# Optimization experiments

Measured on AMD Instinct MI355X. Metric: run time of the kernel, lower is better.

The kernel has to match this reference:

```python
import jax, jax.numpy as jnp
import numpy as np

NEG_INF = -9e15
LEAKY_SLOPE = 0.2  # init alpha
N, IN_DIM, OUT_DIM = 8192, 512, 256


def setup_inputs() -> dict:
    key = jax.random.key(0)
    k1, k2, k3, k4, k5 = jax.random.split(key, 5)
    h = jax.random.normal(k1, (N, IN_DIM), dtype=jnp.float32)
    adj = jax.random.randint(k2, (N, N), 0, 2, dtype=jnp.int32)
    W = jax.random.normal(k3, (IN_DIM, OUT_DIM), dtype=jnp.float32) * 0.06
    a_left = jax.random.normal(k4, (OUT_DIM, 1), dtype=jnp.float32) * 0.1
    a_right = jax.random.normal(k5, (OUT_DIM, 1), dtype=jnp.float32) * 0.1
    return {"h": h, "adj": adj, "W": W, "a_left": a_left, "a_right": a_right}


def reference(h, adj, W, a_left, a_right):
    Wh = h @ W                                  # [N, out_dim]
    Wh1 = Wh @ a_left                           # [N, 1]
    Wh2 = Wh @ a_right                          # [N, 1]
    e = Wh1 + Wh2.T                             # [N, N] broadcast additive scores
    e = jnp.where(e > 0, e, LEAKY_SLOPE * e)    # LeakyReLU
    e = jnp.where(adj > 0, e, NEG_INF)          # adjacency mask
    attention = jax.nn.softmax(e, axis=1)       # row-wise softmax (dropout=0, eval)
    h_out = attention @ Wh                      # [N, out_dim]
    return jax.nn.elu(h_out)                    # activation=True
```

## Files before the change

kernel.cpp:

```cpp
#include <hip/hip_runtime.h>
#include <hip/hip_bf16.h>
#include <cstdint>
#include <cstddef>

typedef float  f32x4  __attribute__((ext_vector_type(4)));
typedef __bf16 bf16x8 __attribute__((ext_vector_type(8)));

#define LOG2E 1.4426950408889634f

static constexpr int GN   = 8192;
static constexpr int GIN  = 512;
static constexpr int GOUT = 256;

static __device__ __forceinline__ void gload_lds16(const void* g, void* lds){
  typedef uint32_t __attribute__((address_space(1)))* gp_t;
  typedef uint32_t __attribute__((address_space(3)))* lp_t;
  __builtin_amdgcn_global_load_lds((gp_t)(uintptr_t)g,
                                   (lp_t)(uint32_t)(uintptr_t)lds, 16, 0, 0);
}

__global__ void k_wa(const float* __restrict__ W, const float* __restrict__ al,
                     const float* __restrict__ ar, float* __restrict__ wal,
                     float* __restrict__ war){
  int k = blockIdx.x;
  int lane = threadIdx.x;
  float4 wv = ((const float4*)(W + (size_t)k*GOUT))[lane];
  float4 av = ((const float4*)al)[lane];
  float4 bv = ((const float4*)ar)[lane];
  float sl = wv.x*av.x + wv.y*av.y + wv.z*av.z + wv.w*av.w;
  float sr = wv.x*bv.x + wv.y*bv.y + wv.z*bv.z + wv.w*bv.w;
  #pragma unroll
  for(int o=32;o;o>>=1){ sl += __shfl_down(sl,o,64); sr += __shfl_down(sr,o,64); }
  if(lane==0){ wal[k] = sl*LOG2E; war[k] = sr*LOG2E; }
}

__global__ void k_prep_h(const float* __restrict__ h, const float* __restrict__ wal,
                         const float* __restrict__ war, __bf16* __restrict__ hb,
                         float* __restrict__ Wh1, float* __restrict__ Wh2){
  int row = blockIdx.x*4 + (threadIdx.x>>6);
  int lane = threadIdx.x & 63;
  const float4* hp = (const float4*)(h + (size_t)row*GIN);
  float4 v0 = hp[lane*2], v1 = hp[lane*2+1];
  bf16x8 o;
  o[0]=(__bf16)v0.x; o[1]=(__bf16)v0.y; o[2]=(__bf16)v0.z; o[3]=(__bf16)v0.w;
  o[4]=(__bf16)v1.x; o[5]=(__bf16)v1.y; o[6]=(__bf16)v1.z; o[7]=(__bf16)v1.w;
  *(bf16x8*)(hb + (size_t)row*GIN + lane*8) = o;
  float4 a0 = ((const float4*)wal)[lane*2], a1 = ((const float4*)wal)[lane*2+1];
  float4 b0 = ((const float4*)war)[lane*2], b1 = ((const float4*)war)[lane*2+1];
  float sl = v0.x*a0.x+v0.y*a0.y+v0.z*a0.z+v0.w*a0.w
           + v1.x*a1.x+v1.y*a1.y+v1.z*a1.z+v1.w*a1.w;
  float sr = v0.x*b0.x+v0.y*b0.y+v0.z*b0.z+v0.w*b0.w
           + v1.x*b1.x+v1.y*b1.y+v1.z*b1.z+v1.w*b1.w;
  #pragma unroll
  for(int of=32;of;of>>=1){ sl += __shfl_down(sl,of,64); sr += __shfl_down(sr,of,64); }
  if(lane==0){ Wh1[row]=sl; Wh2[row]=sr; }
}

__global__ void k_wt(const float* __restrict__ W, __bf16* __restrict__ WT){
  int idx = blockIdx.x*256 + threadIdx.x;
  int k = idx >> 8, c = idx & 255;
  WT[(size_t)c*GIN + k] = (__bf16)W[idx];
}

__global__ __launch_bounds__(256,1) void k_gemmT(const __bf16* __restrict__ WT,
                                                 const __bf16* __restrict__ hb,
                                                 __bf16* __restrict__ WhbT){
  __shared__ __attribute__((aligned(16))) __bf16 As[2][64*64];
  __shared__ __attribute__((aligned(16))) __bf16 Bs[2][128*64];
  const int tid = threadIdx.x, lane = tid & 63, w = tid >> 6;
  const int mb = blockIdx.x >> 6, nb = blockIdx.x & 63;
  const int m0 = mb*64, n0 = nb*128;

  f32x4 acc[8];
  #pragma unroll
  for(int t=0;t<8;t++) acc[t] = (f32x4){0.f,0.f,0.f,0.f};

  const int lr = lane>>3;
  const int bs_sw = ((lane&7)*16) ^ (lr<<4);

  auto stage = [&](int it, int buf){
    const int k0b = it*128;
    #pragma unroll
    for(int s=0;s<6;s++){
      int u = w + s*4;
      const char* src; char* dst;
      if(u < 8){
        int r8 = u*8;
        src = (const char*)(WT + (size_t)(m0 + r8 + lr)*GIN);
        dst = (char*)&As[buf][0] + r8*128;
      } else {
        int r8 = (u-8)*8;
        src = (const char*)(hb + (size_t)(n0 + r8 + lr)*GIN);
        dst = (char*)&Bs[buf][0] + r8*128;
      }
      gload_lds16(src + k0b + bs_sw, dst);
    }
  };

  auto kstep = [&](int kk, int buf){
    const int ko = kk*64 + (lane>>4)*16;
    const int am = 16*w + (lane&15);
    bf16x8 af = *(const bf16x8*)((const char*)&As[buf][0] + am*128 + (ko ^ ((am&7)<<4)));
    #pragma unroll
    for(int t=0;t<8;t++){
      int n = 16*t + (lane&15);
      bf16x8 bf = *(const bf16x8*)((const char*)&Bs[buf][0] + n*128 + (ko ^ ((n&7)<<4)));
      acc[t] = __builtin_amdgcn_mfma_f32_16x16x32_bf16(af, bf, acc[t], 0, 0, 0);
    }
  };

  stage(0,0);
  asm volatile("s_waitcnt vmcnt(0)" ::: "memory");
  __builtin_amdgcn_s_barrier();
  for(int it=0; it<8; it++){
    int buf = it & 1;
    if(it < 7) stage(it+1, buf^1);
    kstep(0, buf);
    kstep(1, buf);
    asm volatile("s_waitcnt vmcnt(0)" ::: "memory");
    __builtin_amdgcn_s_barrier();
  }

  const int mrow = m0 + 16*w + 4*(lane>>4);
  const int nc0  = n0 + (lane&15);
  #pragma unroll
  for(int t=0;t<8;t++){
    #pragma unroll
    for(int r=0;r<4;r++){
      WhbT[(size_t)(mrow + r)*GN + nc0 + 16*t] = (__bf16)acc[t][r];
    }
  }
}

template<bool PART>
__global__ __launch_bounds__(256,2) void k_attn(const int* __restrict__ adj,
                                                const __bf16* __restrict__ WhbT,
                                                const float* __restrict__ Wh1s,
                                                const float* __restrict__ Wh2s,
                                                float* __restrict__ pv_out,
                                                float* __restrict__ s_out){
  __shared__ __attribute__((aligned(16))) __bf16 Vs[2][256*64];
  const int tid = threadIdx.x, lane = tid & 63, w = tid >> 6;
  const int rg = blockIdx.x >> 3, chunk = blockIdx.x & 7;
  const int r0 = rg * 128;
  const int j0 = chunk * 1024;

  f32x4 acc0[16], acc1[16];
  #pragma unroll
  for(int t=0;t<16;t++){ acc0[t] = (f32x4){0.f,0.f,0.f,0.f}; acc1[t] = (f32x4){0.f,0.f,0.f,0.f}; }
  f32x4 accs0 = (f32x4){0.f,0.f,0.f,0.f};
  f32x4 accs1 = (f32x4){0.f,0.f,0.f,0.f};

  bf16x8 ones;
  #pragma unroll
  for(int j=0;j<8;j++) ones[j] = (__bf16)1.0f;

  const int kg  = lane >> 4;
  const int kg8 = kg << 3;
  const int myrow0 = r0 + 16*w + (lane & 15);
  const float wh1_0 = Wh1s[myrow0];
  const float wh1_1 = Wh1s[myrow0 + 64];
  const float* wh2p = Wh2s + j0 + kg8;

  const size_t arow0 = (size_t)(r0 + 16*w) * GN + j0;
  const size_t arow1 = arow0 + (size_t)64 * GN;

  const int lr = lane>>3;
  const int bs_sw = ((lane&7)*16) ^ (lr<<4);

  auto stage = [&](int it, int buf){
    const int colb = (j0 + it*64)*2;
    #pragma unroll
    for(int s=0;s<8;s++){
      int u = w + s*4;
      int r8 = u*8;
      const char* src = (const char*)WhbT + (size_t)(r8 + lr)*(GN*2) + colb + bs_sw;
      gload_lds16(src, (char*)&Vs[buf][0] + r8*128);
    }
  };

  int a0p[16], a1p[16];
  auto adj_load = [&](int tt){
    const int co = tt*64 + lane;
    #pragma unroll
    for(int r=0;r<16;r++) a0p[r] = adj[arow0 + (size_t)r*GN + co];
    #pragma unroll
    for(int r=0;r<16;r++) a1p[r] = adj[arow1 + (size_t)r*GN + co];
  };
  auto adj_pack = [&](uint64_t& m0, uint64_t& m1){
    uint64_t n0 = 0, n1 = 0;
    #pragma unroll
    for(int r=0;r<16;r++){
      uint64_t b = __ballot(a0p[r] != 0);
      if((lane&15)==r) n0 = b;
    }
    #pragma unroll
    for(int r=0;r<16;r++){
      uint64_t b = __ballot(a1p[r] != 0);
      if((lane&15)==r) n1 = b;
    }
    m0 = n0; m1 = n1;
  };

  auto mkpa = [&](float wh1, unsigned m8, float4 w0, float4 w1) -> bf16x8 {
    bf16x8 pa;
    float y, p;
    y = wh1 + w0.x; y = fmaxf(y, 0.2f*y); p = exp2f(y); pa[0] = (__bf16)((m8    )&1 ? p : 0.f);
    y = wh1 + w0.y; y = fmaxf(y, 0.2f*y); p = exp2f(y); pa[1] = (__bf16)((m8>>1)&1 ? p : 0.f);
    y = wh1 + w0.z; y = fmaxf(y, 0.2f*y); p = exp2f(y); pa[2] = (__bf16)((m8>>2)&1 ? p : 0.f);
    y = wh1 + w0.w; y = fmaxf(y, 0.2f*y); p = exp2f(y); pa[3] = (__bf16)((m8>>3)&1 ? p : 0.f);
    y = wh1 + w1.x; y = fmaxf(y, 0.2f*y); p = exp2f(y); pa[4] = (__bf16)((m8>>4)&1 ? p : 0.f);
    y = wh1 + w1.y; y = fmaxf(y, 0.2f*y); p = exp2f(y); pa[5] = (__bf16)((m8>>5)&1 ? p : 0.f);
    y = wh1 + w1.z; y = fmaxf(y, 0.2f*y); p = exp2f(y); pa[6] = (__bf16)((m8>>6)&1 ? p : 0.f);
    y = wh1 + w1.w; y = fmaxf(y, 0.2f*y); p = exp2f(y); pa[7] = (__bf16)((m8>>7)&1 ? p : 0.f);
    return pa;
  };

  uint64_t mk0, mk1;

  auto kstep = [&](int it, int kk, int buf){
    const float* wp = wh2p + it*64 + kk*32;
    float4 w0 = *(const float4*)wp;
    float4 w1 = *(const float4*)(wp + 4);
    unsigned m8_0 = (unsigned)((mk0 >> (kk*32 + kg8)) & 0xffULL);
    unsigned m8_1 = (unsigned)((mk1 >> (kk*32 + kg8)) & 0xffULL);
    bf16x8 pa0 = mkpa(wh1_0, m8_0, w0, w1);
    bf16x8 pa1 = mkpa(wh1_1, m8_1, w0, w1);
    const int ko = kk*64 + kg*16;
    #pragma unroll
    for(int t=0;t<16;t++){
      int n = 16*t + (lane&15);
      bf16x8 bv = *(const bf16x8*)((const char*)&Vs[buf][0] + n*128 + (ko ^ ((n&7)<<4)));
      acc0[t] = __builtin_amdgcn_mfma_f32_16x16x32_bf16(pa0, bv, acc0[t], 0, 0, 0);
      acc1[t] = __builtin_amdgcn_mfma_f32_16x16x32_bf16(pa1, bv, acc1[t], 0, 0, 0);
    }
    accs0 = __builtin_amdgcn_mfma_f32_16x16x32_bf16(pa0, ones, accs0, 0, 0, 0);
    accs1 = __builtin_amdgcn_mfma_f32_16x16x32_bf16(pa1, ones, accs1, 0, 0, 0);
  };

  stage(0, 0);
  adj_load(0);
  adj_pack(mk0, mk1);
  asm volatile("s_waitcnt vmcnt(0)" ::: "memory");
  __builtin_amdgcn_s_barrier();

  for(int it=0; it<16; it++){
    int buf = it & 1;
    if(it < 15){
      stage(it+1, buf^1);
      adj_load(it+1);
    }
    kstep(it, 0, buf);
    kstep(it, 1, buf);
    uint64_t mkn0 = 0, mkn1 = 0;
    if(it < 15) adj_pack(mkn0, mkn1);
    asm volatile("s_waitcnt vmcnt(0)" ::: "memory");
    __builtin_amdgcn_s_barrier();
    mk0 = mkn0; mk1 = mkn1;
  }

  const int orow0 = r0 + 16*w + 4*kg;
  const int orow1 = orow0 + 64;
  const int ocol  = lane & 15;
  if constexpr (PART){
    float* pv = pv_out + (size_t)chunk*GN*GOUT;
    float* sp = s_out  + (size_t)chunk*GN;
    #pragma unroll
    for(int t=0;t<16;t++){
      #pragma unroll
      for(int r=0;r<4;r++){
        pv[(size_t)(orow0 + r)*GOUT + ocol + 16*t] = acc0[t][r];
        pv[(size_t)(orow1 + r)*GOUT + ocol + 16*t] = acc1[t][r];
      }
    }
    if(ocol == 0){
      #pragma unroll
      for(int r=0;r<4;r++){ sp[orow0 + r] = accs0[r]; sp[orow1 + r] = accs1[r]; }
    }
  } else {
    #pragma unroll
    for(int t=0;t<16;t++){
      #pragma unroll
      for(int r=0;r<4;r++){
        atomicAdd(pv_out + (size_t)(orow0 + r)*GOUT + ocol + 16*t, acc0[t][r]);
        atomicAdd(pv_out + (size_t)(orow1 + r)*GOUT + ocol + 16*t, acc1[t][r]);
      }
    }
    if(ocol == 0){
      #pragma unroll
      for(int r=0;r<4;r++){ atomicAdd(s_out + orow0 + r, accs0[r]); atomicAdd(s_out + orow1 + r, accs1[r]); }
    }
  }
}

static __device__ __forceinline__ float elu1(float x){
  return x > 0.f ? x : (exp2f(x*LOG2E) - 1.f);
}

__global__ void k_reduce(const float* __restrict__ accP, const float* __restrict__ accSp,
                         float* __restrict__ out){
  size_t i = ((size_t)blockIdx.x*256 + threadIdx.x)*4;
  int row = (int)(i >> 8);
  float S = 0.f;
  #pragma unroll
  for(int c=0;c<8;c++) S += accSp[(size_t)c*GN + row];
  float4 s = {0.f,0.f,0.f,0.f};
  #pragma unroll
  for(int c=0;c<8;c++){
    float4 v = *(const float4*)(accP + (size_t)c*GN*GOUT + i);
    s.x += v.x; s.y += v.y; s.z += v.z; s.w += v.w;
  }
  float inv = 1.0f / S;
  float4 o;
  o.x = elu1(s.x*inv); o.y = elu1(s.y*inv); o.z = elu1(s.z*inv); o.w = elu1(s.w*inv);
  *(float4*)(out + i) = o;
}

__global__ void k_norm(const float* __restrict__ accPV, const float* __restrict__ accS,
                       float* __restrict__ out){
  size_t i = ((size_t)blockIdx.x*256 + threadIdx.x)*4;
  int row = (int)(i >> 8);
  float inv = 1.0f / accS[row];
  float4 v = *(const float4*)(accPV + i);
  float4 o;
  o.x = elu1(v.x*inv); o.y = elu1(v.y*inv); o.z = elu1(v.z*inv); o.w = elu1(v.w*inv);
  *(float4*)(out + i) = o;
}

extern "C" void kernel_launch(void* const* d_in, const int* in_sizes, int n_in,
                              void* d_out, int out_size, void* d_ws, size_t ws_size,
                              hipStream_t stream){
  const float* h  = (const float*)d_in[0];
  const int*   adj= (const int*)  d_in[1];
  const float* W  = (const float*)d_in[2];
  const float* al = (const float*)d_in[3];
  const float* ar = (const float*)d_in[4];
  float* out = (float*)d_out;
  char* ws = (char*)d_ws;

  const size_t SZ_ACCP = (size_t)8*GN*GOUT*4;
  const size_t NEED_A  = SZ_ACCP + 4194304 + 32768 + 32768 + 262144;

  if(ws_size >= NEED_A){
    float*  accP  = (float*) (ws);
    __bf16* hb    = (__bf16*)(ws);
    __bf16* WT    = (__bf16*)(ws + 8388608);
    float*  wal   = (float*) (ws + 8650752);
    float*  war   = (float*) (ws + 8652800);
    __bf16* WhbT  = (__bf16*)(ws + SZ_ACCP);
    float*  Wh1   = (float*) (ws + SZ_ACCP + 4194304);
    float*  Wh2   = (float*) (ws + SZ_ACCP + 4227072);
    float*  accSp = (float*) (ws + SZ_ACCP + 4259840);

    k_wa    <<<512, 64, 0, stream>>>(W, al, ar, wal, war);
    k_prep_h<<<2048, 256, 0, stream>>>(h, wal, war, hb, Wh1, Wh2);
    k_wt    <<<512, 256, 0, stream>>>(W, WT);
    k_gemmT <<<256, 256, 0, stream>>>(WT, hb, WhbT);
    k_attn<true><<<512, 256, 0, stream>>>(adj, WhbT, Wh1, Wh2, accP, accSp);
    k_reduce<<<2048, 256, 0, stream>>>(accP, accSp, out);
  } else {
    float*  accPV = (float*) (ws);
    float*  accS  = (float*) (ws + 8388608);
    __bf16* hb    = (__bf16*)(ws + 8421376);
    __bf16* WT    = (__bf16*)(ws + 16809984);
    __bf16* WhbT  = (__bf16*)(ws + 17072128);
    float*  wal   = (float*) (ws + 21266432);
    float*  war   = (float*) (ws + 21268480);
    float*  Wh1   = (float*) (ws + 21270528);
    float*  Wh2   = (float*) (ws + 21303296);
    if(ws_size < 21336064) return;

    hipMemsetAsync(accPV, 0, 8388608 + 32768, stream);
    k_wa    <<<512, 64, 0, stream>>>(W, al, ar, wal, war);
    k_prep_h<<<2048, 256, 0, stream>>>(h, wal, war, hb, Wh1, Wh2);
    k_wt    <<<512, 256, 0, stream>>>(W, WT);
    k_gemmT <<<256, 256, 0, stream>>>(WT, hb, WhbT);
    k_attn<false><<<512, 256, 0, stream>>>(adj, WhbT, Wh1, Wh2, accPV, accS);
    k_norm  <<<2048, 256, 0, stream>>>(accPV, accS, out);
  }
}
```

Before: 138.6 us.

## Restructure attention kernel to 2-wave blocks with 32-column K steps and fuse W transpose

The attention kernel moves from 256-thread blocks covering 128 rows with 64-column K tiles to 128-thread blocks covering 64 rows with 32-column K tiles, doubling the grid to 1024 blocks and halving shared memory per block. Adjacency masks now come from 16 ballots per step, with per-lane bit selection replacing the per-row ballot loop. The W transpose-to-bf16 kernel is folded into the W·a prep kernel, removing one launch. The smaller blocks should raise occupancy and simplify mask packing, but they also mean twice as many barrier-synchronised iterations and less reuse of each staged V tile across rows.

Result: slower. 175.7 us (+26.8%).

```diff
diff --git a/kernel.cpp b/kernel.cpp
--- a/kernel.cpp
+++ b/kernel.cpp
@@ -19,14 +19,18 @@
                                    (lp_t)(uint32_t)(uintptr_t)lds, 16, 0, 0);
 }
 
-__global__ void k_wa(const float* __restrict__ W, const float* __restrict__ al,
-                     const float* __restrict__ ar, float* __restrict__ wal,
-                     float* __restrict__ war){
+__global__ void k_wprep(const float* __restrict__ W, const float* __restrict__ al,
+                        const float* __restrict__ ar, float* __restrict__ wal,
+                        float* __restrict__ war, __bf16* __restrict__ WT){
   int k = blockIdx.x;
   int lane = threadIdx.x;
   float4 wv = ((const float4*)(W + (size_t)k*GOUT))[lane];
   float4 av = ((const float4*)al)[lane];
   float4 bv = ((const float4*)ar)[lane];
+  WT[(size_t)(lane*4+0)*GIN + k] = (__bf16)wv.x;
+  WT[(size_t)(lane*4+1)*GIN + k] = (__bf16)wv.y;
+  WT[(size_t)(lane*4+2)*GIN + k] = (__bf16)wv.z;
+  WT[(size_t)(lane*4+3)*GIN + k] = (__bf16)wv.w;
   float sl = wv.x*av.x + wv.y*av.y + wv.z*av.z + wv.w*av.w;
   float sr = wv.x*bv.x + wv.y*bv.y + wv.z*bv.z + wv.w*bv.w;
   #pragma unroll
@@ -56,12 +60,6 @@
   if(lane==0){ Wh1[row]=sl; Wh2[row]=sr; }
 }
 
-__global__ void k_wt(const float* __restrict__ W, __bf16* __restrict__ WT){
-  int idx = blockIdx.x*256 + threadIdx.x;
-  int k = idx >> 8, c = idx & 255;
-  WT[(size_t)c*GIN + k] = (__bf16)W[idx];
-}
-
 __global__ __launch_bounds__(256,1) void k_gemmT(const __bf16* __restrict__ WT,
                                                  const __bf16* __restrict__ hb,
                                                  __bf16* __restrict__ WhbT){
@@ -133,17 +131,18 @@
 }
 
 template<bool PART>
-__global__ __launch_bounds__(256,2) void k_attn(const int* __restrict__ adj,
+__global__ __launch_bounds__(128,2) void k_attn(const int* __restrict__ adj,
                                                 const __bf16* __restrict__ WhbT,
                                                 const float* __restrict__ Wh1s,
                                                 const float* __restrict__ Wh2s,
                                                 float* __restrict__ pv_out,
                                                 float* __restrict__ s_out){
-  __shared__ __attribute__((aligned(16))) __bf16 Vs[2][256*64];
-  const int tid = threadIdx.x, lane = tid & 63, w = tid >> 6;
+  __shared__ __attribute__((aligned(16))) char Vs[2][16384];
+  const int tid = threadIdx.x, lane = tid & 63, wv = tid >> 6;
   const int rg = blockIdx.x >> 3, chunk = blockIdx.x & 7;
-  const int r0 = rg * 128;
-  const int j0 = chunk * 1024;
+  const int r0 = rg*64, wrb = r0 + wv*32;
+  const int j0 = chunk*1024;
+  const int la = lane & 15, kg = lane >> 4, kg8 = kg*8;
 
   f32x4 acc0[16], acc1[16];
   #pragma unroll
@@ -155,51 +154,51 @@
   #pragma unroll
   for(int j=0;j<8;j++) ones[j] = (__bf16)1.0f;
 
-  const int kg  = lane >> 4;
-  const int kg8 = kg << 3;
-  const int myrow0 = r0 + 16*w + (lane & 15);
-  const float wh1_0 = Wh1s[myrow0];
-  const float wh1_1 = Wh1s[myrow0 + 64];
-  const float* wh2p = Wh2s + j0 + kg8;
-
-  const size_t arow0 = (size_t)(r0 + 16*w) * GN + j0;
-  const size_t arow1 = arow0 + (size_t)64 * GN;
-
-  const int lr = lane>>3;
-  const int bs_sw = ((lane&7)*16) ^ (lr<<4);
+  const float wh1_0 = Wh1s[wrb + la];
+  const float wh1_1 = Wh1s[wrb + 16 + la];
+
+  const size_t vsrc_off = (size_t)(wv*16 + (lane>>2))*(GN*2)
+                        + (size_t)(((lane&3) ^ ((lane>>3)&3)) << 4);
+  const size_t abase = (size_t)(wrb + (lane>>5))*GN + j0 + (lane&31);
+
+  int ax[16];
+  uint64_t bc[16];
+  auto adj_load = [&](int it){
+    const size_t o = abase + it*32;
+    #pragma unroll
+    for(int l=0;l<16;l++) ax[l] = adj[o + (size_t)(2*l)*GN];
+  };
+  auto adj_pack = [&](){
+    #pragma unroll
+    for(int l=0;l<16;l++) bc[l] = __ballot(ax[l] != 0);
+  };
 
   auto stage = [&](int it, int buf){
-    const int colb = (j0 + it*64)*2;
+    const size_t jt2 = (size_t)(j0 + it*32)*2;
+    const char* src0 = (const char*)WhbT + jt2 + vsrc_off;
+    char* dst0 = &Vs[buf][0] + wv*1024;
     #pragma unroll
     for(int s=0;s<8;s++){
-      int u = w + s*4;
-      int r8 = u*8;
-      const char* src = (const char*)WhbT + (size_t)(r8 + lr)*(GN*2) + colb + bs_sw;
-      gload_lds16(src, (char*)&Vs[buf][0] + r8*128);
-    }
-  };
-
-  int a0p[16], a1p[16];
-  auto adj_load = [&](int tt){
-    const int co = tt*64 + lane;
-    #pragma unroll
-    for(int r=0;r<16;r++) a0p[r] = adj[arow0 + (size_t)r*GN + co];
-    #pragma unroll
-    for(int r=0;r<16;r++) a1p[r] = adj[arow1 + (size_t)r*GN + co];
-  };
-  auto adj_pack = [&](uint64_t& m0, uint64_t& m1){
-    uint64_t n0 = 0, n1 = 0;
-    #pragma unroll
-    for(int r=0;r<16;r++){
-      uint64_t b = __ballot(a0p[r] != 0);
-      if((lane&15)==r) n0 = b;
-    }
-    #pragma unroll
-    for(int r=0;r<16;r++){
-      uint64_t b = __ballot(a1p[r] != 0);
-      if((lane&15)==r) n1 = b;
-    }
-    m0 = n0; m1 = n1;
+      gload_lds16(src0 + (size_t)s*32*(GN*2), dst0 + s*2048);
+    }
+  };
+
+  const unsigned odd = lane & 1;
+  const unsigned sel = (lane >> 1) & 7;
+  auto pick = [&](int base)->unsigned{
+    uint32_t h0 = odd ? (uint32_t)(bc[base+0]>>32) : (uint32_t)bc[base+0];
+    uint32_t h1 = odd ? (uint32_t)(bc[base+1]>>32) : (uint32_t)bc[base+1];
+    uint32_t h2 = odd ? (uint32_t)(bc[base+2]>>32) : (uint32_t)bc[base+2];
+    uint32_t h3 = odd ? (uint32_t)(bc[base+3]>>32) : (uint32_t)bc[base+3];
+    uint32_t h4 = odd ? (uint32_t)(bc[base+4]>>32) : (uint32_t)bc[base+4];
+    uint32_t h5 = odd ? (uint32_t)(bc[base+5]>>32) : (uint32_t)bc[base+5];
+    uint32_t h6 = odd ? (uint32_t)(bc[base+6]>>32) : (uint32_t)bc[base+6];
+    uint32_t h7 = odd ? (uint32_t)(bc[base+7]>>32) : (uint32_t)bc[base+7];
+    uint32_t u01 = (sel&1)? h1:h0, u23 = (sel&1)? h3:h2;
+    uint32_t u45 = (sel&1)? h5:h4, u67 = (sel&1)? h7:h6;
+    uint32_t v03 = (sel&2)? u23:u01, v47 = (sel&2)? u67:u45;
+    uint32_t m32 = (sel&4)? v47:v03;
+    return (m32 >> kg8) & 0xffu;
   };
 
   auto mkpa = [&](float wh1, unsigned m8, float4 w0, float4 w1) -> bf16x8 {
@@ -216,21 +215,18 @@
     return pa;
   };
 
-  uint64_t mk0, mk1;
-
-  auto kstep = [&](int it, int kk, int buf){
-    const float* wp = wh2p + it*64 + kk*32;
+  auto kstep = [&](int it, int buf){
+    const float* wp = Wh2s + j0 + it*32 + kg8;
     float4 w0 = *(const float4*)wp;
     float4 w1 = *(const float4*)(wp + 4);
-    unsigned m8_0 = (unsigned)((mk0 >> (kk*32 + kg8)) & 0xffULL);
-    unsigned m8_1 = (unsigned)((mk1 >> (kk*32 + kg8)) & 0xffULL);
+    unsigned m8_0 = pick(0);
+    unsigned m8_1 = pick(8);
     bf16x8 pa0 = mkpa(wh1_0, m8_0, w0, w1);
     bf16x8 pa1 = mkpa(wh1_1, m8_1, w0, w1);
-    const int ko = kk*64 + kg*16;
+    const char* vb = &Vs[buf][0] + la*64 + 16*(kg ^ ((la>>1)&3));
     #pragma unroll
     for(int t=0;t<16;t++){
-      int n = 16*t + (lane&15);
-      bf16x8 bv = *(const bf16x8*)((const char*)&Vs[buf][0] + n*128 + (ko ^ ((n&7)<<4)));
+      bf16x8 bv = *(const bf16x8*)(vb + 1024*t);
       acc0[t] = __builtin_amdgcn_mfma_f32_16x16x32_bf16(pa0, bv, acc0[t], 0, 0, 0);
       acc1[t] = __builtin_amdgcn_mfma_f32_16x16x32_bf16(pa1, bv, acc1[t], 0, 0, 0);
     }
@@ -240,28 +236,25 @@
 
   stage(0, 0);
   adj_load(0);
-  adj_pack(mk0, mk1);
+  adj_pack();
   asm volatile("s_waitcnt vmcnt(0)" ::: "memory");
   __builtin_amdgcn_s_barrier();
 
-  for(int it=0; it<16; it++){
+  for(int it=0; it<32; it++){
     int buf = it & 1;
-    if(it < 15){
+    if(it < 31){
       stage(it+1, buf^1);
       adj_load(it+1);
     }
-    kstep(it, 0, buf);
-    kstep(it, 1, buf);
-    uint64_t mkn0 = 0, mkn1 = 0;
-    if(it < 15) adj_pack(mkn0, mkn1);
+    kstep(it, buf);
+    if(it < 31) adj_pack();
     asm volatile("s_waitcnt vmcnt(0)" ::: "memory");
     __builtin_amdgcn_s_barrier();
-    mk0 = mkn0; mk1 = mkn1;
-  }
-
-  const int orow0 = r0 + 16*w + 4*kg;
-  const int orow1 = orow0 + 64;
-  const int ocol  = lane & 15;
+  }
+
+  const int orow0 = wrb + 4*kg;
+  const int orow1 = wrb + 16 + 4*kg;
+  const int ocol  = la;
   if constexpr (PART){
     float* pv = pv_out + (size_t)chunk*GN*GOUT;
     float* sp = s_out  + (size_t)chunk*GN;
@@ -352,11 +345,10 @@
     float*  Wh2   = (float*) (ws + SZ_ACCP + 4227072);
     float*  accSp = (float*) (ws + SZ_ACCP + 4259840);
 
-    k_wa    <<<512, 64, 0, stream>>>(W, al, ar, wal, war);
+    k_wprep <<<512, 64, 0, stream>>>(W, al, ar, wal, war, WT);
     k_prep_h<<<2048, 256, 0, stream>>>(h, wal, war, hb, Wh1, Wh2);
-    k_wt    <<<512, 256, 0, stream>>>(W, WT);
     k_gemmT <<<256, 256, 0, stream>>>(WT, hb, WhbT);
-    k_attn<true><<<512, 256, 0, stream>>>(adj, WhbT, Wh1, Wh2, accP, accSp);
+    k_attn<true><<<1024, 128, 0, stream>>>(adj, WhbT, Wh1, Wh2, accP, accSp);
     k_reduce<<<2048, 256, 0, stream>>>(accP, accSp, out);
   } else {
     float*  accPV = (float*) (ws);
@@ -371,11 +363,10 @@
     if(ws_size < 21336064) return;
 
     hipMemsetAsync(accPV, 0, 8388608 + 32768, stream);
-    k_wa    <<<512, 64, 0, stream>>>(W, al, ar, wal, war);
+    k_wprep <<<512, 64, 0, stream>>>(W, al, ar, wal, war, WT);
     k_prep_h<<<2048, 256, 0, stream>>>(h, wal, war, hb, Wh1, Wh2);
-    k_wt    <<<512, 256, 0, stream>>>(W, WT);
     k_gemmT <<<256, 256, 0, stream>>>(WT, hb, WhbT);
-    k_attn<false><<<512, 256, 0, stream>>>(adj, WhbT, Wh1, Wh2, accPV, accS);
+    k_attn<false><<<1024, 128, 0, stream>>>(adj, WhbT, Wh1, Wh2, accPV, accS);
     k_norm  <<<2048, 256, 0, stream>>>(accPV, accS, out);
   }
 }
```
